# Kernel optimization log

Hardware: AMD Instinct MI355X
Metric: run time of the kernel (lower is better)

## Reference

```python
import jax, jax.numpy as jnp
import numpy as np
from functools import partial

HID = 16
EMB = 32

def setup_inputs() -> dict:
    key = jax.random.key(0)
    ks = jax.random.split(key, 9)
    S, B, V = 64, 32, 50257
    stdv = 1.0 / np.sqrt(HID)
    u = lambda k, shp: jax.random.uniform(k, shp, jnp.float32, -stdv, stdv)
    return {
        "input_batch": jax.random.randint(ks[0], (S, B), 0, V),
        "embedding": u(ks[1], (V, EMB)),  # original re-inits randn embedding with uniform via init_params
        "W_lr": u(ks[2], (HID, EMB + HID)),
        "b_lr": u(ks[3], (HID,)),
        "W_rl": u(ks[4], (HID, EMB + HID)),
        "b_rl": u(ks[5], (HID,)),
        "W_ho": u(ks[6], (V, 2 * HID)),
        "b_ho": u(ks[7], (V,)),
        "h0": u(ks[8], (1, HID)),
    }


def _rnn_pre_states(emb, W, b, h0):
    # emb: [S,B,E]; returns stacked hidden states BEFORE each step: [S,B,H]
    def step(h, x):
        h_new = jnp.tanh(jnp.concatenate([x, h], axis=-1) @ W.T + b)
        return h_new, h  # collect pre-update state
    _, pre = jax.lax.scan(step, h0, emb)
    return pre


def reference(input_batch, embedding, W_lr, b_lr, W_rl, b_rl, W_ho, b_ho, h0):
    S, B = input_batch.shape
    emb = embedding[input_batch]                      # [S,B,EMB]
    h0b = jnp.broadcast_to(h0, (B, HID))
    # Left-to-right: prediction at i uses hLR state before consuming word i
    hLR_pre = _rnn_pre_states(emb, W_lr, b_lr, h0b)   # [S,B,HID]
    # Right-to-left: run over reversed sequence, collect pre-states, reverse back
    hRL_pre = _rnn_pre_states(emb[::-1], W_rl, b_rl, h0b)[::-1]  # [S,B,HID]
    h = jnp.concatenate([hLR_pre, hRL_pre], axis=-1)  # [S,B,2*HID]
    logits = jnp.einsum('sbh,vh->sbv', h, W_ho) + b_ho
    return jax.nn.log_softmax(logits, axis=-1)        # [S,B,V]
```

## Files before the change

### kernel.cpp

```cpp
#include <hip/hip_runtime.h>
#include <hip/hip_bf16.h>

#define S 64
#define B 32
#define HID 16
#define EMB 32
#define V 50257
#define NCB 197
#define VP2 (NCB*256)
#define M 2048
#define PREP_BLOCKS (VP2*EMB/256)
#define NRG 4
#define RT_PER (128/NRG)
#define NRG2 8
#define RT2 (128/NRG2)

using bf16x8 = __attribute__((ext_vector_type(8))) __bf16;
using f32x4  = __attribute__((ext_vector_type(4))) float;

__global__ void k_prep(const float* __restrict__ W_ho, const float* __restrict__ b_ho,
                       const int* __restrict__ idx, const float* __restrict__ emb,
                       const float* __restrict__ W_lr, const float* __restrict__ b_lr,
                       const float* __restrict__ W_rl, const float* __restrict__ b_rl,
                       __bf16* __restrict__ Wb, float* __restrict__ bias,
                       float* __restrict__ P) {
    const int bx = blockIdx.x;
    if (bx < PREP_BLOCKS) {
        int i = bx * 256 + threadIdx.x;
        if (i < VP2) bias[i] = (i < V) ? b_ho[i] : -1e30f;
        int v = i >> 5;
        Wb[i] = (v < V) ? (__bf16)W_ho[i] : (__bf16)0.f;
    } else {
        int i = (bx - PREP_BLOCKS) * 256 + threadIdx.x;
        const int dir = i >> 15, r = i & 32767, m = r >> 4, j = r & 15;
        const float* W  = dir ? W_rl : W_lr;
        const float* bb = dir ? b_rl : b_lr;
        const int tok = idx[m];
        const float4* er = reinterpret_cast<const float4*>(emb + (size_t)tok * EMB);
        const float4* wr = reinterpret_cast<const float4*>(W + j * (EMB + HID));
        float acc = bb[j];
        #pragma unroll
        for (int q = 0; q < 8; ++q) {
            float4 e4 = er[q], w4 = wr[q];
            acc += e4.x * w4.x + e4.y * w4.y + e4.z * w4.z + e4.w * w4.w;
        }
        P[i] = acc;
    }
}

__global__ void k_rnn(const float* __restrict__ P,
                      const float* __restrict__ W_lr, const float* __restrict__ W_rl,
                      const float* __restrict__ h0, __bf16* __restrict__ hcat) {
    __shared__ float Psh[S * 4 * HID];
    __shared__ float hsh[4][17];
    const int t = threadIdx.x;
    const int dir = blockIdx.x >> 3, bq = blockIdx.x & 7;
    const int bl = t >> 4, j = t & 15;
    const int b = bq * 4 + bl;
    {
        const float4* Pg4 = reinterpret_cast<const float4*>(P);
        float4* Ps4 = reinterpret_cast<float4*>(Psh);
        #pragma unroll
        for (int i = 0; i < 16; ++i) {
            int s = (t >> 4) + 4 * i;
            Ps4[t + 64 * i] = Pg4[dir * 8192 + s * 128 + bq * 16 + (t & 15)];
        }
    }
    const float* Wd = (dir ? W_rl : W_lr) + j * (EMB + HID) + EMB;
    float wh[16];
    #pragma unroll
    for (int q = 0; q < 4; ++q) {
        float4 w4 = *reinterpret_cast<const float4*>(Wd + q * 4);
        wh[q * 4 + 0] = w4.x; wh[q * 4 + 1] = w4.y;
        wh[q * 4 + 2] = w4.z; wh[q * 4 + 3] = w4.w;
    }
    float hcur = h0[j];
    hsh[bl][j] = hcur;
    for (int step = 0; step < S; ++step) {
        const int s = dir ? (S - 1 - step) : step;
        hcat[(s * B + b) * 32 + dir * HID + j] = (__bf16)hcur;
        float acc = Psh[s * 64 + bl * 16 + j];
        #pragma unroll
        for (int k = 0; k < HID; ++k) acc += wh[k] * hsh[bl][k];
        hcur = tanhf(acc);
        hsh[bl][j] = hcur;
    }
}

__global__ void k_pass1(const __bf16* __restrict__ hb, const __bf16* __restrict__ Wb,
                        const float* __restrict__ bias, float* __restrict__ partials) {
    const int cbx = blockIdx.x, rg = blockIdx.y;
    const int wave = threadIdx.x >> 6, lane = threadIdx.x & 63;
    const int lr = lane & 15, kg = lane >> 4;
    const int ttbase = cbx * 16 + wave * 4;
    bf16x8 wfrag[4]; float bc[4];
    #pragma unroll
    for (int q = 0; q < 4; ++q) {
        wfrag[q] = *reinterpret_cast<const bf16x8*>(Wb + ((ttbase + q) * 16 + lr) * 32 + kg * 8);
        bc[q] = bias[(ttbase + q) * 16 + lr];
    }
    __shared__ float red[4][16];
    const f32x4 zero = {0.f, 0.f, 0.f, 0.f};
    for (int rt = rg * RT_PER; rt < rg * RT_PER + RT_PER; ++rt) {
        const int m0 = rt * 16;
        const bf16x8 a = *reinterpret_cast<const bf16x8*>(hb + (m0 + lr) * 32 + kg * 8);
        float s0 = 0.f, s1 = 0.f, s2 = 0.f, s3 = 0.f;
        #pragma unroll
        for (int q = 0; q < 4; ++q) {
            f32x4 d = __builtin_amdgcn_mfma_f32_16x16x32_bf16(a, wfrag[q], zero, 0, 0, 0);
            s0 += __expf(d[0] + bc[q]);
            s1 += __expf(d[1] + bc[q]);
            s2 += __expf(d[2] + bc[q]);
            s3 += __expf(d[3] + bc[q]);
        }
        #pragma unroll
        for (int off = 1; off < 16; off <<= 1) {
            s0 += __shfl_xor(s0, off);
            s1 += __shfl_xor(s1, off);
            s2 += __shfl_xor(s2, off);
            s3 += __shfl_xor(s3, off);
        }
        if (lr == 0) {
            red[wave][kg * 4 + 0] = s0;
            red[wave][kg * 4 + 1] = s1;
            red[wave][kg * 4 + 2] = s2;
            red[wave][kg * 4 + 3] = s3;
        }
        __syncthreads();
        if (threadIdx.x < 16)
            partials[cbx * M + m0 + threadIdx.x] =
                red[0][threadIdx.x] + red[1][threadIdx.x] +
                red[2][threadIdx.x] + red[3][threadIdx.x];
        __syncthreads();
    }
}

__global__ void k_reduce(const float* __restrict__ partials, float* __restrict__ logZ) {
    int r = blockIdx.x * 256 + threadIdx.x;
    float tot = 0.f;
    for (int c = 0; c < NCB; ++c) tot += partials[c * M + r];
    logZ[r] = logf(tot);
}

__global__ void k_pass2(const __bf16* __restrict__ hb, const __bf16* __restrict__ Wb,
                        const float* __restrict__ bias, const float* __restrict__ logZ,
                        float* __restrict__ out) {
    __shared__ float stage[4][16][68];
    const int cbx = blockIdx.x, rg = blockIdx.y;
    const int wave = threadIdx.x >> 6, lane = threadIdx.x & 63;
    const int lr = lane & 15, kg = lane >> 4;
    const int ttbase = cbx * 16 + wave * 4;
    bf16x8 wfrag[4]; float bc[4];
    #pragma unroll
    for (int q = 0; q < 4; ++q) {
        wfrag[q] = *reinterpret_cast<const bf16x8*>(Wb + ((ttbase + q) * 16 + lr) * 32 + kg * 8);
        bc[q] = bias[(ttbase + q) * 16 + lr];
    }
    float (*st)[68] = stage[wave];
    const int cb0 = cbx * 256 + wave * 64;
    const int nv = V - cb0;
    const f32x4 zero = {0.f, 0.f, 0.f, 0.f};
    for (int rt = rg * RT2; rt < rg * RT2 + RT2; ++rt) {
        const int m0 = rt * 16;
        const bf16x8 a = *reinterpret_cast<const bf16x8*>(hb + (m0 + lr) * 32 + kg * 8);
        #pragma unroll
        for (int q = 0; q < 4; ++q) {
            f32x4 d = __builtin_amdgcn_mfma_f32_16x16x32_bf16(a, wfrag[q], zero, 0, 0, 0);
            const int cl = q * 16 + lr;
            #pragma unroll
            for (int r = 0; r < 4; ++r)
                st[kg * 4 + r][cl] = d[r] + bc[q];
        }
        asm volatile("s_waitcnt lgkmcnt(0)" ::: "memory");
        __builtin_amdgcn_sched_barrier(0);
        #pragma unroll
        for (int r = 0; r < 16; ++r) {
            const int m = m0 + r;
            const float lz = logZ[m];
            if (lane < nv)
                out[(size_t)m * V + cb0 + lane] = st[r][lane] - lz;
        }
        asm volatile("s_waitcnt lgkmcnt(0)" ::: "memory");
        __builtin_amdgcn_sched_barrier(0);
    }
}

extern "C" void kernel_launch(void* const* d_in, const int* in_sizes, int n_in,
                              void* d_out, int out_size, void* d_ws, size_t ws_size,
                              hipStream_t stream) {
    const int*   idx       = (const int*)d_in[0];
    const float* embedding = (const float*)d_in[1];
    const float* W_lr      = (const float*)d_in[2];
    const float* b_lr      = (const float*)d_in[3];
    const float* W_rl      = (const float*)d_in[4];
    const float* b_rl      = (const float*)d_in[5];
    const float* W_ho      = (const float*)d_in[6];
    const float* b_ho      = (const float*)d_in[7];
    const float* h0        = (const float*)d_in[8];
    float* out = (float*)d_out;

    char* ws = (char*)d_ws;
    size_t off = 0;
    __bf16* Wb      = (__bf16*)(ws + off); off += (size_t)VP2 * EMB * 2;
    float*  bias    = (float*)(ws + off);  off += (size_t)VP2 * 4;
    __bf16* hb      = (__bf16*)(ws + off); off += (size_t)M * 32 * 2;
    float*  P       = (float*)(ws + off);  off += (size_t)2 * M * HID * 4;
    float*  partials= (float*)(ws + off);  off += (size_t)NCB * M * 4;
    float*  logZ    = (float*)(ws + off);  off += (size_t)M * 4;

    k_prep<<<PREP_BLOCKS + 256, 256, 0, stream>>>(W_ho, b_ho, idx, embedding,
                                                  W_lr, b_lr, W_rl, b_rl, Wb, bias, P);
    k_rnn<<<16, 64, 0, stream>>>(P, W_lr, W_rl, h0, hb);
    k_pass1<<<dim3(NCB, NRG), 256, 0, stream>>>(hb, Wb, bias, partials);
    k_reduce<<<8, 256, 0, stream>>>(partials, logZ);
    k_pass2<<<dim3(NCB, NRG2), 256, 0, stream>>>(hb, Wb, bias, logZ, out);
}
```

Before: 208.0 us.

## Restructure pass2 grid to one row tile per block and shuffle RNN state

The output-writing kernel now launches one block per 16-row tile and group of three column blocks, instead of looping over row tiles with persistent weight fragments. It folds the logZ subtraction into the LDS staging and moves the bounds check so only the last column group pays for it. The RNN kernel replaces the shared-memory hidden-state exchange with wavefront shuffles, and pass1 uses more row groups. This trades weight-fragment reuse across row tiles for many more blocks and more parallelism in the write-bound output stage.

```diff
diff --git a/kernel.cpp b/kernel.cpp
--- a/kernel.cpp
+++ b/kernel.cpp
@@ -7,13 +7,13 @@
 #define EMB 32
 #define V 50257
 #define NCB 197
-#define VP2 (NCB*256)
+#define NCG2 66
+#define CPG2 3
+#define VP5 (NCG2*CPG2*256)
 #define M 2048
-#define PREP_BLOCKS (VP2*EMB/256)
-#define NRG 4
+#define PREP_BLOCKS (VP5*EMB/256)
+#define NRG 8
 #define RT_PER (128/NRG)
-#define NRG2 8
-#define RT2 (128/NRG2)
 
 using bf16x8 = __attribute__((ext_vector_type(8))) __bf16;
 using f32x4  = __attribute__((ext_vector_type(4))) float;
@@ -27,7 +27,7 @@
     const int bx = blockIdx.x;
     if (bx < PREP_BLOCKS) {
         int i = bx * 256 + threadIdx.x;
-        if (i < VP2) bias[i] = (i < V) ? b_ho[i] : -1e30f;
+        if (i < VP5) bias[i] = (i < V) ? b_ho[i] : -1e30f;
         int v = i >> 5;
         Wb[i] = (v < V) ? (__bf16)W_ho[i] : (__bf16)0.f;
     } else {
@@ -52,7 +52,6 @@
                       const float* __restrict__ W_lr, const float* __restrict__ W_rl,
                       const float* __restrict__ h0, __bf16* __restrict__ hcat) {
     __shared__ float Psh[S * 4 * HID];
-    __shared__ float hsh[4][17];
     const int t = threadIdx.x;
     const int dir = blockIdx.x >> 3, bq = blockIdx.x & 7;
     const int bl = t >> 4, j = t & 15;
@@ -75,15 +74,14 @@
         wh[q * 4 + 2] = w4.z; wh[q * 4 + 3] = w4.w;
     }
     float hcur = h0[j];
-    hsh[bl][j] = hcur;
     for (int step = 0; step < S; ++step) {
         const int s = dir ? (S - 1 - step) : step;
         hcat[(s * B + b) * 32 + dir * HID + j] = (__bf16)hcur;
         float acc = Psh[s * 64 + bl * 16 + j];
         #pragma unroll
-        for (int k = 0; k < HID; ++k) acc += wh[k] * hsh[bl][k];
+        for (int k = 0; k < HID; ++k)
+            acc += wh[k] * __shfl(hcur, (t & 48) + k, 64);
         hcur = tanhf(acc);
-        hsh[bl][j] = hcur;
     }
 }
 
@@ -139,49 +137,64 @@
     int r = blockIdx.x * 256 + threadIdx.x;
     float tot = 0.f;
     for (int c = 0; c < NCB; ++c) tot += partials[c * M + r];
-    logZ[r] = logf(tot);
-}
-
-__global__ void k_pass2(const __bf16* __restrict__ hb, const __bf16* __restrict__ Wb,
-                        const float* __restrict__ bias, const float* __restrict__ logZ,
-                        float* __restrict__ out) {
-    __shared__ float stage[4][16][68];
-    const int cbx = blockIdx.x, rg = blockIdx.y;
-    const int wave = threadIdx.x >> 6, lane = threadIdx.x & 63;
+    logZ[r] = __logf(tot);
+}
+
+__global__ __launch_bounds__(256, 4) void k_pass2(
+        const __bf16* __restrict__ hb, const __bf16* __restrict__ Wb,
+        const float* __restrict__ bias, const float* __restrict__ logZ,
+        float* __restrict__ out) {
+    __shared__ float stg[4][16][68];
+    const int cg = blockIdx.x, rt = blockIdx.y;
+    const int t = threadIdx.x;
+    const int m0 = rt * 16;
+    const int wave = t >> 6, lane = t & 63;
     const int lr = lane & 15, kg = lane >> 4;
-    const int ttbase = cbx * 16 + wave * 4;
-    bf16x8 wfrag[4]; float bc[4];
-    #pragma unroll
-    for (int q = 0; q < 4; ++q) {
-        wfrag[q] = *reinterpret_cast<const bf16x8*>(Wb + ((ttbase + q) * 16 + lr) * 32 + kg * 8);
-        bc[q] = bias[(ttbase + q) * 16 + lr];
-    }
-    float (*st)[68] = stage[wave];
-    const int cb0 = cbx * 256 + wave * 64;
-    const int nv = V - cb0;
+    const int c0 = cg * CPG2;
+
+    const bf16x8 a = *reinterpret_cast<const bf16x8*>(hb + (m0 + lr) * 32 + kg * 8);
+    float lzr[4];
+    #pragma unroll
+    for (int r = 0; r < 4; ++r) lzr[r] = logZ[m0 + kg * 4 + r];
+    bf16x8 wf[CPG2][4];
+    float  bc[CPG2][4];
+    #pragma unroll
+    for (int c = 0; c < CPG2; ++c) {
+        const int t0 = (c0 + c) * 16 + wave * 4;
+        #pragma unroll
+        for (int q = 0; q < 4; ++q) {
+            wf[c][q] = *reinterpret_cast<const bf16x8*>(Wb + ((t0 + q) * 16 + lr) * 32 + kg * 8);
+            bc[c][q] = bias[(t0 + q) * 16 + lr];
+        }
+    }
+    float (*st)[68] = stg[wave];
+    const bool guard = (cg == NCG2 - 1);
     const f32x4 zero = {0.f, 0.f, 0.f, 0.f};
-    for (int rt = rg * RT2; rt < rg * RT2 + RT2; ++rt) {
-        const int m0 = rt * 16;
-        const bf16x8 a = *reinterpret_cast<const bf16x8*>(hb + (m0 + lr) * 32 + kg * 8);
+
+    #pragma unroll
+    for (int c = 0; c < CPG2; ++c) {
         #pragma unroll
         for (int q = 0; q < 4; ++q) {
-            f32x4 d = __builtin_amdgcn_mfma_f32_16x16x32_bf16(a, wfrag[q], zero, 0, 0, 0);
+            f32x4 d = __builtin_amdgcn_mfma_f32_16x16x32_bf16(a, wf[c][q], zero, 0, 0, 0);
             const int cl = q * 16 + lr;
             #pragma unroll
             for (int r = 0; r < 4; ++r)
-                st[kg * 4 + r][cl] = d[r] + bc[q];
+                st[kg * 4 + r][cl] = d[r] + bc[c][q] - lzr[r];
         }
         asm volatile("s_waitcnt lgkmcnt(0)" ::: "memory");
         __builtin_amdgcn_sched_barrier(0);
-        #pragma unroll
-        for (int r = 0; r < 16; ++r) {
-            const int m = m0 + r;
-            const float lz = logZ[m];
-            if (lane < nv)
-                out[(size_t)m * V + cb0 + lane] = st[r][lane] - lz;
-        }
-        asm volatile("s_waitcnt lgkmcnt(0)" ::: "memory");
-        __builtin_amdgcn_sched_barrier(0);
+        const int cb0 = (c0 + c) * 256 + wave * 64;
+        const int vcol = cb0 + lane;
+        float* p = out + (size_t)m0 * V + vcol;
+        if (!guard) {
+            #pragma unroll
+            for (int r = 0; r < 16; ++r)
+                p[(size_t)r * V] = st[r][lane];
+        } else {
+            #pragma unroll
+            for (int r = 0; r < 16; ++r)
+                if (vcol < V) p[(size_t)r * V] = st[r][lane];
+        }
     }
 }
 
@@ -201,8 +214,8 @@
 
     char* ws = (char*)d_ws;
     size_t off = 0;
-    __bf16* Wb      = (__bf16*)(ws + off); off += (size_t)VP2 * EMB * 2;
-    float*  bias    = (float*)(ws + off);  off += (size_t)VP2 * 4;
+    __bf16* Wb      = (__bf16*)(ws + off); off += (size_t)VP5 * EMB * 2;
+    float*  bias    = (float*)(ws + off);  off += (size_t)VP5 * 4;
     __bf16* hb      = (__bf16*)(ws + off); off += (size_t)M * 32 * 2;
     float*  P       = (float*)(ws + off);  off += (size_t)2 * M * HID * 4;
     float*  partials= (float*)(ws + off);  off += (size_t)NCB * M * 4;
@@ -213,5 +226,5 @@
     k_rnn<<<16, 64, 0, stream>>>(P, W_lr, W_rl, h0, hb);
     k_pass1<<<dim3(NCB, NRG), 256, 0, stream>>>(hb, Wb, bias, partials);
     k_reduce<<<8, 256, 0, stream>>>(partials, logZ);
-    k_pass2<<<dim3(NCB, NRG2), 256, 0, stream>>>(hb, Wb, bias, logZ, out);
-}
+    k_pass2<<<dim3(NCG2, 128), 256, 0, stream>>>(hb, Wb, bias, logZ, out);
+}
```

Result: faster. 188.3 us (-9.5%).
